# Kernel optimization log

Measured on AMD Instinct MI355X. Metric: run time of the kernel, lower is better.

The kernel has to match this reference:

```python
import jax, jax.numpy as jnp
import numpy as np

EPS = 1e-6  # ieps_ln_default
B, S, H, DI, DO = 4, 4096, 8, 128, 128


def _ln(x, g, b, n_axes):
    """LayerNorm over the last n_axes dims (matches nn.LayerNorm(normalized_shape))."""
    axes = tuple(range(x.ndim - n_axes, x.ndim))
    mu = x.mean(axes, keepdims=True)
    var = x.var(axes, keepdims=True)
    return (x - mu) * jax.lax.rsqrt(var + EPS) * g + b


def setup_inputs() -> dict:
    key = jax.random.key(0)
    ks = jax.random.split(key, 12)
    sd = 0.02
    return {
        "heads_input": jax.random.normal(ks[0], (B, S, H, DI), jnp.float32),
        # GroupLinear trans_hid: per-head (2*DI -> 3*DO)
        "W_hid": jax.random.normal(ks[1], (H, 2 * DI, 3 * DO), jnp.float32) * sd,
        "b_hid": jnp.zeros((H, 3 * DO), jnp.float32),
        # normer_csum LN over (H, DI)
        "g_csum": jnp.ones((H, DI), jnp.float32),
        "beta_csum": jnp.zeros((H, DI), jnp.float32),
        # normer_hid LN over (H, 3, DO)
        "g_hid": jnp.ones((H, 3, DO), jnp.float32),
        "beta_hid": jnp.zeros((H, 3, DO), jnp.float32),
        # GroupLinear trans_og: per-head (DI + DO -> DO)
        "W_og": jax.random.normal(ks[2], (H, DI + DO, DO), jnp.float32) * sd,
        "b_og": jnp.zeros((H, DO), jnp.float32),
        # LN inside trans_og over (H, DO)
        "g_og": jnp.ones((H, DO), jnp.float32),
        "beta_og": jnp.zeros((H, DO), jnp.float32),
        "init_cx": jnp.zeros((H, DO), jnp.float32),
    }


def reference(heads_input, W_hid, b_hid, g_csum, beta_csum, g_hid, beta_hid,
              W_og, b_og, g_og, beta_og, init_cx):
    b, s, n, d = heads_input.shape
    # exclusive cumulative sum over seq: cat(zeros, x[:, :-1]).cumsum(1)
    csum = jnp.cumsum(heads_input, axis=1) - heads_input
    csum = _ln(csum, g_csum, beta_csum, 2)
    # grouped (per-head) linear producing igate/fgate/hidden
    x = jnp.concatenate([heads_input, csum], axis=-1)              # [b,s,n,2*d]
    h3 = jnp.einsum('bsni,nio->bsno', x, W_hid) + b_hid            # [b,s,n,3*do]
    do = h3.shape[-1] // 3
    h3 = _ln(h3.reshape(b, s, n, 3, do), g_hid, beta_hid, 3)
    igate, fgate, hidden = h3[..., 0, :], h3[..., 1, :], h3[..., 2, :]
    fg = jax.nn.sigmoid(fgate)
    igh = jax.nn.sigmoid(igate) * jax.nn.relu(hidden)
    # linear recurrence cell_t = fg_t * cell_{t-1} + igh_t  (LGateFunc, dim=1)
    c0 = jnp.broadcast_to(init_cx, (b, n, do))

    def step(c, fi):
        f, i = fi
        c = f * c + i
        return c, c

    _, cell = jax.lax.scan(step, c0, (jnp.swapaxes(fg, 0, 1), jnp.swapaxes(igh, 0, 1)))
    cell = jnp.swapaxes(cell, 0, 1)                                # [b,s,n,do]
    # output gate: GroupLinear + LN, then sigmoid * cell
    og_in = jnp.concatenate([heads_input, cell], axis=-1)
    og = jnp.einsum('bsni,nio->bsno', og_in, W_og) + b_og
    og = _ln(og, g_og, beta_og, 2)
    return jax.nn.sigmoid(og) * cell
```

## Files before the change

### kernel.cpp

```cpp
#include <hip/hip_runtime.h>
#include <math.h>

#define BB 4
#define SS 4096
#define HH 8
#define DI 128
#define DOo 128
#define HD 1024
#define NTOK (BB*SS)
#define LNEPS 1e-6f

#define CS1 64
#define NC1 64
#define CS2 128
#define NC2 32

typedef unsigned short ubf;
typedef __attribute__((ext_vector_type(8))) short    bf16x8;
typedef __attribute__((ext_vector_type(8))) unsigned short u16x8;
typedef __attribute__((ext_vector_type(4))) unsigned short u16x4;
typedef __attribute__((ext_vector_type(4))) float    f32x4;

__device__ __forceinline__ float bf2f(ubf x) {
    union { unsigned int u; float f; } v; v.u = ((unsigned int)x) << 16; return v.f;
}
__device__ __forceinline__ ubf f2bf(float f) {
    union { float f; unsigned int u; } v; v.f = f;
    unsigned int r = v.u + 0x7FFFu + ((v.u >> 16) & 1u);
    return (ubf)(r >> 16);
}
__device__ __forceinline__ float fast_sigmoid(float x) {
    return __builtin_amdgcn_rcpf(1.f + __expf(-x));
}
__device__ __forceinline__ void gload16(const ubf* g, ubf* l) {
    __builtin_amdgcn_global_load_lds(
        (const __attribute__((address_space(1))) void*)g,
        (__attribute__((address_space(3))) void*)l, 16, 0, 0);
}

__global__ void kwt_pack(const float* __restrict__ W, ubf* __restrict__ Wtp, int NB) {
    int bid = blockIdx.x;
    int ks = bid & 7;
    int ns = (bid >> 3) % (NB >> 6);
    int h  = bid / (8 * (NB >> 6));
    int t = threadIdx.x;
    int j = t >> 6, lane = t & 63;
    int n  = ns * 64 + j * 16 + (lane & 15);
    int k0 = ks * 32 + (lane >> 4) * 8;
    u16x8 o;
    #pragma unroll
    for (int e = 0; e < 8; ++e)
        o[e] = f2bf(W[((size_t)h * 256 + k0 + e) * NB + n]);
    *(u16x8*)(Wtp + ((((size_t)(h * (NB >> 6) + ns) * 8 + ks) * 4 + j) * 64 + lane) * 8) = o;
}

__global__ void k1_chunksum(const float* __restrict__ in, float* __restrict__ chunk,
                            ubf* __restrict__ in_bf) {
    int bid = blockIdx.x;
    int c = bid % NC1;
    int h = (bid / NC1) % HH;
    int b = bid / (NC1 * HH);
    int d = threadIdx.x;
    size_t base = (size_t)(b * SS + c * CS1) * HD + h * DI + d;
    float s = 0.f;
    for (int i = 0; i < CS1; ++i) {
        float v = in[base + (size_t)i * HD];
        in_bf[base + (size_t)i * HD] = f2bf(v);
        s += v;
    }
    chunk[((b * NC1 + c) * HH + h) * DI + d] = s;
}

__global__ void k2_chunkscan(float* __restrict__ chunk) {
    int bid = blockIdx.x;
    int h = bid % HH;
    int b = bid / HH;
    int d = threadIdx.x;
    float run = 0.f;
    for (int c = 0; c < NC1; ++c) {
        int idx = ((b * NC1 + c) * HH + h) * DI + d;
        float v = chunk[idx];
        chunk[idx] = run;
        run += v;
    }
}

__global__ void __launch_bounds__(256) k3_csum_ln(
        const float* __restrict__ in, const float* __restrict__ chunkpre,
        const float* __restrict__ g, const float* __restrict__ beta,
        ubf* __restrict__ out) {
    __shared__ float2 scr[2][4];
    int c = blockIdx.x % NC1;
    int b = blockIdx.x / NC1;
    int t = threadIdx.x;
    int lane = t & 63, w = t >> 6;
    int d0 = t * 4;
    f32x4 run = *(const f32x4*)(chunkpre + (size_t)(b * NC1 + c) * HD + d0);
    f32x4 gg  = *(const f32x4*)(g + d0);
    f32x4 bb  = *(const f32x4*)(beta + d0);
    const float* pin = in + (size_t)(b * SS + c * CS1) * HD + d0;
    ubf* pout = out + (size_t)(b * SS + c * CS1) * HD + d0;

    f32x4 v = *(const f32x4*)(pin);
    for (int i = 0; i < CS1; ++i) {
        f32x4 cs = run;
        run += v;
        float s = cs[0] + cs[1] + cs[2] + cs[3];
        float q = cs[0]*cs[0] + cs[1]*cs[1] + cs[2]*cs[2] + cs[3]*cs[3];
        #pragma unroll
        for (int off = 32; off >= 1; off >>= 1) {
            s += __shfl_xor(s, off);
            q += __shfl_xor(q, off);
        }
        if (lane == 0) scr[i & 1][w] = make_float2(s, q);
        if (i + 1 < CS1) v = *(const f32x4*)(pin + (size_t)(i + 1) * HD);
        __syncthreads();
        float2 p0 = scr[i & 1][0], p1 = scr[i & 1][1];
        float2 p2 = scr[i & 1][2], p3 = scr[i & 1][3];
        float S = p0.x + p1.x + p2.x + p3.x;
        float Q = p0.y + p1.y + p2.y + p3.y;
        float mu = S * (1.f / 1024.f);
        float r = rsqrtf(Q * (1.f / 1024.f) - mu * mu + LNEPS);
        u16x4 o;
        #pragma unroll
        for (int e = 0; e < 4; ++e) o[e] = f2bf((cs[e] - mu) * r * gg[e] + bb[e]);
        *(u16x4*)(pout + (size_t)i * HD) = o;
    }
}

__global__ void __launch_bounds__(256, 2) gemm_h(
        const ubf* __restrict__ Ab0, const ubf* __restrict__ Ab1,
        const ubf* __restrict__ Wtp, const float* __restrict__ bias,
        ubf* __restrict__ C, int NB) {
    __shared__ __align__(16) ubf As[64 * 512];
    int t = threadIdx.x;
    int lane = t & 63, w = t >> 6;
    int h = blockIdx.x & 7;
    int tok0 = (blockIdx.x >> 3) * 128;
    int ntiles = NB >> 7;
    int crs = NB * HH;
    int rl = lane & 15, kq = lane >> 4;

    {
        int rowi = lane >> 4;
        int cg = (lane & 15) ^ rowi;
        #pragma unroll
        for (int q = 0; q < 16; ++q) {
            int bi = w * 16 + q;
            int rowgrp = bi >> 1, half = bi & 1;
            int row = rowgrp * 4 + rowi;
            const ubf* src = (half ? Ab1 : Ab0)
                             + (size_t)(tok0 + row) * HD + h * DI + cg * 8;
            gload16(src, As + bi * 512);
        }
    }
    __syncthreads();

    const ubf* pWb = Wtp + ((size_t)h * (NB >> 6)) * 16384 + (size_t)lane * 8;

    for (int nt = 0; nt < ntiles; ++nt) {
        int ns = nt * 2 + (w >> 1);
        f32x4 acc[4][4];
        #pragma unroll
        for (int i = 0; i < 4; ++i)
            #pragma unroll
            for (int j = 0; j < 4; ++j) acc[i][j] = (f32x4){0.f, 0.f, 0.f, 0.f};

        #pragma unroll
        for (int ks = 0; ks < 8; ++ks) {
            bf16x8 bfr[4], af[4];
            #pragma unroll
            for (int j = 0; j < 4; ++j)
                bfr[j] = *(const bf16x8*)(pWb + (size_t)((ns * 8 + ks) * 4 + j) * 512);
            int c = ks * 4 + kq;
            int chi = (c >> 4) * 512;
            int clo = ((c & 15) ^ (rl & 3)) * 8;
            #pragma unroll
            for (int i = 0; i < 4; ++i) {
                int r = (w & 1) * 64 + i * 16 + rl;
                af[i] = *(const bf16x8*)(As + ((r >> 2) * 2) * 512 + chi
                                            + (r & 3) * 128 + clo);
            }
            #pragma unroll
            for (int i = 0; i < 4; ++i)
                #pragma unroll
                for (int j = 0; j < 4; ++j)
                    acc[i][j] = __builtin_amdgcn_mfma_f32_16x16x32_bf16(bfr[j], af[i], acc[i][j], 0, 0, 0);
        }

        int nq0 = nt * 128 + (w >> 1) * 64 + kq * 4;
        #pragma unroll
        for (int j = 0; j < 4; ++j) {
            int n = nq0 + j * 16;
            f32x4 bv = *(const f32x4*)(bias + h * NB + n);
            int col = (n >> 7) * 1024 + h * 128 + (n & 127);
            #pragma unroll
            for (int i = 0; i < 4; ++i) {
                u16x4 o;
                o[0] = f2bf(acc[i][j][0] + bv[0]);
                o[1] = f2bf(acc[i][j][1] + bv[1]);
                o[2] = f2bf(acc[i][j][2] + bv[2]);
                o[3] = f2bf(acc[i][j][3] + bv[3]);
                *(u16x4*)(C + (size_t)(tok0 + (w & 1) * 64 + i * 16 + rl) * crs + col) = o;
            }
        }
    }
}

__global__ void __launch_bounds__(256, 4) k4b_ln_gates(
        const ubf* __restrict__ h3, const float* __restrict__ g,
        const float* __restrict__ beta, ubf* __restrict__ fgl, float* __restrict__ igh) {
    int lane = threadIdx.x & 63;
    int tok  = blockIdx.x * 4 + (threadIdx.x >> 6);
    int c0 = 8 * lane;
    const ubf* p = h3 + (size_t)tok * 3072;

    u16x8 raw[6];
    #pragma unroll
    for (int pp = 0; pp < 3; ++pp) {
        raw[pp * 2 + 0] = *(const u16x8*)(p + pp * 1024 + c0);
        raw[pp * 2 + 1] = *(const u16x8*)(p + pp * 1024 + 512 + c0);
    }
    float sum = 0.f, sq = 0.f;
    #pragma unroll
    for (int s = 0; s < 6; ++s) {
        #pragma unroll
        for (int j = 0; j < 8; ++j) {
            float a = bf2f((ubf)raw[s][j]);
            sum += a; sq = fmaf(a, a, sq);
        }
    }
    #pragma unroll
    for (int m = 32; m >= 1; m >>= 1) {
        sum += __shfl_xor(sum, m);
        sq  += __shfl_xor(sq, m);
    }
    float mu = sum * (1.f / 3072.f);
    float r  = rsqrtf(sq * (1.f / 3072.f) - mu * mu + LNEPS);

    int dd = c0 & 127;
    size_t ob = (size_t)tok * HD + c0;
    #pragma unroll
    for (int q = 0; q < 2; ++q) {
        int hq = (c0 + q * 512) >> 7;
        int gb = hq * 384 + dd;
        f32x4 gv[3][2], bv[3][2];
        #pragma unroll
        for (int pp = 0; pp < 3; ++pp) {
            gv[pp][0] = *(const f32x4*)(g + gb + pp * 128);
            gv[pp][1] = *(const f32x4*)(g + gb + pp * 128 + 4);
            bv[pp][0] = *(const f32x4*)(beta + gb + pp * 128);
            bv[pp][1] = *(const f32x4*)(beta + gb + pp * 128 + 4);
        }
        u16x8 fo;
        f32x4 io0, io1;
        #pragma unroll
        for (int j = 0; j < 8; ++j) {
            float ai = bf2f((ubf)raw[0 + q][j]);
            float af = bf2f((ubf)raw[2 + q][j]);
            float ah = bf2f((ubf)raw[4 + q][j]);
            float li = (ai - mu) * r * gv[0][j >> 2][j & 3] + bv[0][j >> 2][j & 3];
            float lf = (af - mu) * r * gv[1][j >> 2][j & 3] + bv[1][j >> 2][j & 3];
            float lh = (ah - mu) * r * gv[2][j >> 2][j & 3] + bv[2][j >> 2][j & 3];
            fo[j] = f2bf(lf);
            float v = fast_sigmoid(li) * fmaxf(lh, 0.f);
            if (j < 4) io0[j & 3] = v; else io1[j & 3] = v;
        }
        *(u16x8*)(fgl + ob + q * 512) = fo;
        *(f32x4*)(igh + ob + q * 512) = io0;
        *(f32x4*)(igh + ob + q * 512 + 4) = io1;
    }
}

__global__ void k5a_chunkrec(const ubf* __restrict__ fgl, const float* __restrict__ igh,
                             float* __restrict__ Pb, float* __restrict__ Lb) {
    int bid = blockIdx.x;
    int h = bid % HH;
    int c = (bid / HH) % NC2;
    int b = bid / (HH * NC2);
    int d = threadIdx.x;
    size_t base = (size_t)(b * SS + c * CS2) * HD + h * DOo + d;
    float P = 1.f, L = 0.f;
    for (int s = 0; s < CS2; ++s) {
        float f = 1.f / (1.f + expf(-bf2f(fgl[base + (size_t)s * HD])));
        float i = igh[base + (size_t)s * HD];
        L = f * L + i;
        P *= f;
    }
    int o = ((b * NC2 + c) * HH + h) * DOo + d;
    Pb[o] = P;
    Lb[o] = L;
}

__global__ void k5b_carry(const float* __restrict__ Pb, const float* __restrict__ Lb,
                          const float* __restrict__ init_cx, float* __restrict__ cIn) {
    int bid = blockIdx.x;
    int h = bid % HH;
    int b = bid / HH;
    int d = threadIdx.x;
    float c = init_cx[h * DOo + d];
    for (int cc = 0; cc < NC2; ++cc) {
        int o = ((b * NC2 + cc) * HH + h) * DOo + d;
        cIn[o] = c;
        c = Pb[o] * c + Lb[o];
    }
}

__global__ void k5c_cell(const ubf* __restrict__ fgl, float* __restrict__ igh_cell,
                         const float* __restrict__ cIn, ubf* __restrict__ cell_bf) {
    int bid = blockIdx.x;
    int h = bid % HH;
    int c = (bid / HH) % NC2;
    int b = bid / (HH * NC2);
    int d = threadIdx.x;
    size_t base = (size_t)(b * SS + c * CS2) * HD + h * DOo + d;
    int o = ((b * NC2 + c) * HH + h) * DOo + d;
    float cv = cIn[o];
    for (int s = 0; s < CS2; ++s) {
        float f = 1.f / (1.f + expf(-bf2f(fgl[base + (size_t)s * HD])));
        float i = igh_cell[base + (size_t)s * HD];
        cv = f * cv + i;
        igh_cell[base + (size_t)s * HD] = cv;
        cell_bf[base + (size_t)s * HD] = f2bf(cv);
    }
}

__global__ void __launch_bounds__(256, 4) k6b_ln_out(
        const ubf* __restrict__ ogr, float* __restrict__ out ,
        const float* __restrict__ g, const float* __restrict__ beta) {
    int lane = threadIdx.x & 63;
    int tok  = blockIdx.x * 4 + (threadIdx.x >> 6);
    int c0 = 8 * lane;
    size_t base = (size_t)tok * HD + c0;

    u16x8 og0 = *(const u16x8*)(ogr + base);
    u16x8 og1 = *(const u16x8*)(ogr + base + 512);
    f32x4 cl[2][2];
    cl[0][0] = *(const f32x4*)(out + base);
    cl[0][1] = *(const f32x4*)(out + base + 4);
    cl[1][0] = *(const f32x4*)(out + base + 512);
    cl[1][1] = *(const f32x4*)(out + base + 512 + 4);

    float sum = 0.f, sq = 0.f;
    #pragma unroll
    for (int j = 0; j < 8; ++j) {
        float a0 = bf2f((ubf)og0[j]);
        float a1 = bf2f((ubf)og1[j]);
        sum += a0 + a1;
        sq = fmaf(a0, a0, sq);
        sq = fmaf(a1, a1, sq);
    }
    #pragma unroll
    for (int m = 32; m >= 1; m >>= 1) {
        sum += __shfl_xor(sum, m);
        sq  += __shfl_xor(sq, m);
    }
    float mu = sum * (1.f / 1024.f);
    float r  = rsqrtf(sq * (1.f / 1024.f) - mu * mu + LNEPS);

    #pragma unroll
    for (int q = 0; q < 2; ++q) {
        f32x4 gv0 = *(const f32x4*)(g + q * 512 + c0);
        f32x4 gv1 = *(const f32x4*)(g + q * 512 + c0 + 4);
        f32x4 bv0 = *(const f32x4*)(beta + q * 512 + c0);
        f32x4 bv1 = *(const f32x4*)(beta + q * 512 + c0 + 4);
        f32x4 o0, o1;
        #pragma unroll
        for (int j = 0; j < 8; ++j) {
            float a = bf2f((ubf)(q ? og1[j] : og0[j]));
            float gg = (j < 4) ? gv0[j & 3] : gv1[j & 3];
            float bb = (j < 4) ? bv0[j & 3] : bv1[j & 3];
            float lo = (a - mu) * r * gg + bb;
            float v = fast_sigmoid(lo) * cl[q][j >> 2][j & 3];
            if (j < 4) o0[j & 3] = v; else o1[j & 3] = v;
        }
        *(f32x4*)(out + base + q * 512) = o0;
        *(f32x4*)(out + base + q * 512 + 4) = o1;
    }
}

extern "C" void kernel_launch(void* const* d_in, const int* in_sizes, int n_in,
                              void* d_out, int out_size, void* d_ws, size_t ws_size,
                              hipStream_t stream) {
    const float* heads_input = (const float*)d_in[0];
    const float* W_hid   = (const float*)d_in[1];
    const float* b_hid   = (const float*)d_in[2];
    const float* g_csum  = (const float*)d_in[3];
    const float* beta_csum = (const float*)d_in[4];
    const float* g_hid   = (const float*)d_in[5];
    const float* beta_hid = (const float*)d_in[6];
    const float* W_og    = (const float*)d_in[7];
    const float* b_og    = (const float*)d_in[8];
    const float* g_og    = (const float*)d_in[9];
    const float* beta_og = (const float*)d_in[10];
    const float* init_cx = (const float*)d_in[11];
    float* out = (float*)d_out;

    char* ws = (char*)d_ws;
    ubf* in_bf   = (ubf*)ws;
    ubf* csln_bf = (ubf*)(ws + (size_t)33554432);
    ubf* big     = (ubf*)(ws + (size_t)67108864);
    ubf* h3      = big;
    ubf* cell_bf = big;
    ubf* og_bf   = big + (size_t)NTOK * HD;
    char* tail   = ws + (size_t)167772160;
    float* chunk = (float*)tail;
    float* Pb    = chunk + (size_t)BB * NC1 * HD;
    float* Lb    = Pb + (size_t)BB * NC2 * HD;
    float* cIn   = Lb + (size_t)BB * NC2 * HD;
    ubf* Wt_hid  = (ubf*)(cIn + (size_t)BB * NC2 * HD);
    ubf* Wt_og   = Wt_hid + (size_t)HH * 384 * 256;
    ubf* fgl     = csln_bf;

    kwt_pack<<<HH * (384 >> 6) * 8, 256, 0, stream>>>(W_hid, Wt_hid, 384);
    kwt_pack<<<HH * (128 >> 6) * 8, 256, 0, stream>>>(W_og, Wt_og, 128);
    k1_chunksum<<<BB * HH * NC1, 128, 0, stream>>>(heads_input, chunk, in_bf);
    k2_chunkscan<<<BB * HH, 128, 0, stream>>>(chunk);
    k3_csum_ln<<<BB * NC1, 256, 0, stream>>>(heads_input, chunk, g_csum, beta_csum, csln_bf);
    gemm_h<<<(NTOK / 128) * HH, 256, 0, stream>>>(in_bf, csln_bf, Wt_hid, b_hid, h3, 384);
    k4b_ln_gates<<<NTOK / 4, 256, 0, stream>>>(h3, g_hid, beta_hid, fgl, out);
    k5a_chunkrec<<<BB * NC2 * HH, 128, 0, stream>>>(fgl, out, Pb, Lb);
    k5b_carry<<<BB * HH, 128, 0, stream>>>(Pb, Lb, init_cx, cIn);
    k5c_cell<<<BB * NC2 * HH, 128, 0, stream>>>(fgl, out, cIn, cell_bf);
    gemm_h<<<(NTOK / 128) * HH, 256, 0, stream>>>(in_bf, cell_bf, Wt_og, b_og, og_bf, 128);
    k6b_ln_out<<<NTOK / 4, 256, 0, stream>>>(og_bf, out, g_og, beta_og);
}
```

Before: 422.6 us.

## Halve csum chunk size, batch scan loads, prefetch GEMM weights, add LDS swizzle

Changes the csum chunk size from 64 to 32 tokens to double the parallelism of the chunk-sum and LN kernels. The serial chunk-scan and carry kernels now batch their loads into registers before the dependent loop, to hide global latency. The GEMM is templated on N so the tile loop unrolls, preloads all B fragments for a tile up front, and applies an extra XOR swizzle on the LDS A tile to cut bank conflicts. The chunk buffer moves into the big workspace region, which is safe because it is dead before h3 is written. Preloading all B fragments raises register pressure and may reduce occupancy.

```diff
diff --git a/kernel.cpp b/kernel.cpp
--- a/kernel.cpp
+++ b/kernel.cpp
@@ -10,8 +10,8 @@
 #define NTOK (BB*SS)
 #define LNEPS 1e-6f
 
-#define CS1 64
-#define NC1 64
+#define CS1 32
+#define NC1 128
 #define CS2 128
 #define NC2 32
 
@@ -77,11 +77,17 @@
     int b = bid / HH;
     int d = threadIdx.x;
     float run = 0.f;
-    for (int c = 0; c < NC1; ++c) {
-        int idx = ((b * NC1 + c) * HH + h) * DI + d;
-        float v = chunk[idx];
-        chunk[idx] = run;
-        run += v;
+    for (int c0 = 0; c0 < NC1; c0 += 16) {
+        float v[16];
+        #pragma unroll
+        for (int k = 0; k < 16; ++k)
+            v[k] = chunk[((b * NC1 + c0 + k) * HH + h) * DI + d];
+        #pragma unroll
+        for (int k = 0; k < 16; ++k) {
+            int idx = ((b * NC1 + c0 + k) * HH + h) * DI + d;
+            chunk[idx] = run;
+            run += v[k];
+        }
     }
 }
 
@@ -128,27 +134,28 @@
     }
 }
 
+template <int NB>
 __global__ void __launch_bounds__(256, 2) gemm_h(
         const ubf* __restrict__ Ab0, const ubf* __restrict__ Ab1,
         const ubf* __restrict__ Wtp, const float* __restrict__ bias,
-        ubf* __restrict__ C, int NB) {
+        ubf* __restrict__ C) {
     __shared__ __align__(16) ubf As[64 * 512];
+    constexpr int ntiles = NB >> 7;
     int t = threadIdx.x;
     int lane = t & 63, w = t >> 6;
     int h = blockIdx.x & 7;
     int tok0 = (blockIdx.x >> 3) * 128;
-    int ntiles = NB >> 7;
     int crs = NB * HH;
     int rl = lane & 15, kq = lane >> 4;
 
     {
         int rowi = lane >> 4;
-        int cg = (lane & 15) ^ rowi;
         #pragma unroll
         for (int q = 0; q < 16; ++q) {
             int bi = w * 16 + q;
             int rowgrp = bi >> 1, half = bi & 1;
             int row = rowgrp * 4 + rowi;
+            int cg = (lane & 15) ^ rowi ^ ((rowgrp & 3) << 2);
             const ubf* src = (half ? Ab1 : Ab0)
                              + (size_t)(tok0 + row) * HD + h * DI + cg * 8;
             gload16(src, As + bi * 512);
@@ -158,8 +165,16 @@
 
     const ubf* pWb = Wtp + ((size_t)h * (NB >> 6)) * 16384 + (size_t)lane * 8;
 
+    #pragma unroll
     for (int nt = 0; nt < ntiles; ++nt) {
         int ns = nt * 2 + (w >> 1);
+        bf16x8 bfr[8][4];
+        #pragma unroll
+        for (int ks = 0; ks < 8; ++ks)
+            #pragma unroll
+            for (int j = 0; j < 4; ++j)
+                bfr[ks][j] = *(const bf16x8*)(pWb + (size_t)((ns * 8 + ks) * 4 + j) * 512);
+
         f32x4 acc[4][4];
         #pragma unroll
         for (int i = 0; i < 4; ++i)
@@ -168,13 +183,10 @@
 
         #pragma unroll
         for (int ks = 0; ks < 8; ++ks) {
-            bf16x8 bfr[4], af[4];
-            #pragma unroll
-            for (int j = 0; j < 4; ++j)
-                bfr[j] = *(const bf16x8*)(pWb + (size_t)((ns * 8 + ks) * 4 + j) * 512);
             int c = ks * 4 + kq;
             int chi = (c >> 4) * 512;
-            int clo = ((c & 15) ^ (rl & 3)) * 8;
+            int clo = (((c & 15) ^ (rl & 3)) ^ (((rl >> 2) & 3) << 2)) * 8;
+            bf16x8 af[4];
             #pragma unroll
             for (int i = 0; i < 4; ++i) {
                 int r = (w & 1) * 64 + i * 16 + rl;
@@ -185,7 +197,7 @@
             for (int i = 0; i < 4; ++i)
                 #pragma unroll
                 for (int j = 0; j < 4; ++j)
-                    acc[i][j] = __builtin_amdgcn_mfma_f32_16x16x32_bf16(bfr[j], af[i], acc[i][j], 0, 0, 0);
+                    acc[i][j] = __builtin_amdgcn_mfma_f32_16x16x32_bf16(bfr[ks][j], af[i], acc[i][j], 0, 0, 0);
         }
 
         int nq0 = nt * 128 + (w >> 1) * 64 + kq * 4;
@@ -299,10 +311,20 @@
     int b = bid / HH;
     int d = threadIdx.x;
     float c = init_cx[h * DOo + d];
-    for (int cc = 0; cc < NC2; ++cc) {
-        int o = ((b * NC2 + cc) * HH + h) * DOo + d;
-        cIn[o] = c;
-        c = Pb[o] * c + Lb[o];
+    for (int c0 = 0; c0 < NC2; c0 += 8) {
+        float pv[8], lv[8];
+        #pragma unroll
+        for (int k = 0; k < 8; ++k) {
+            int o = ((b * NC2 + c0 + k) * HH + h) * DOo + d;
+            pv[k] = Pb[o];
+            lv[k] = Lb[o];
+        }
+        #pragma unroll
+        for (int k = 0; k < 8; ++k) {
+            int o = ((b * NC2 + c0 + k) * HH + h) * DOo + d;
+            cIn[o] = c;
+            c = pv[k] * c + lv[k];
+        }
     }
 }
 
@@ -400,12 +422,12 @@
     ubf* in_bf   = (ubf*)ws;
     ubf* csln_bf = (ubf*)(ws + (size_t)33554432);
     ubf* big     = (ubf*)(ws + (size_t)67108864);
+    float* chunk = (float*)big;
     ubf* h3      = big;
     ubf* cell_bf = big;
     ubf* og_bf   = big + (size_t)NTOK * HD;
     char* tail   = ws + (size_t)167772160;
-    float* chunk = (float*)tail;
-    float* Pb    = chunk + (size_t)BB * NC1 * HD;
+    float* Pb    = (float*)tail;
     float* Lb    = Pb + (size_t)BB * NC2 * HD;
     float* cIn   = Lb + (size_t)BB * NC2 * HD;
     ubf* Wt_hid  = (ubf*)(cIn + (size_t)BB * NC2 * HD);
@@ -417,11 +439,11 @@
     k1_chunksum<<<BB * HH * NC1, 128, 0, stream>>>(heads_input, chunk, in_bf);
     k2_chunkscan<<<BB * HH, 128, 0, stream>>>(chunk);
     k3_csum_ln<<<BB * NC1, 256, 0, stream>>>(heads_input, chunk, g_csum, beta_csum, csln_bf);
-    gemm_h<<<(NTOK / 128) * HH, 256, 0, stream>>>(in_bf, csln_bf, Wt_hid, b_hid, h3, 384);
+    gemm_h<384><<<(NTOK / 128) * HH, 256, 0, stream>>>(in_bf, csln_bf, Wt_hid, b_hid, h3);
     k4b_ln_gates<<<NTOK / 4, 256, 0, stream>>>(h3, g_hid, beta_hid, fgl, out);
     k5a_chunkrec<<<BB * NC2 * HH, 128, 0, stream>>>(fgl, out, Pb, Lb);
     k5b_carry<<<BB * HH, 128, 0, stream>>>(Pb, Lb, init_cx, cIn);
     k5c_cell<<<BB * NC2 * HH, 128, 0, stream>>>(fgl, out, cIn, cell_bf);
-    gemm_h<<<(NTOK / 128) * HH, 256, 0, stream>>>(in_bf, cell_bf, Wt_og, b_og, og_bf, 128);
+    gemm_h<128><<<(NTOK / 128) * HH, 256, 0, stream>>>(in_bf, cell_bf, Wt_og, b_og, og_bf);
     k6b_ln_out<<<NTOK / 4, 256, 0, stream>>>(og_bf, out, g_og, beta_og);
 }
```

New measurement: 407.6 us. -3.6%, faster.
